# Kernel optimization log

Hardware: AMD Instinct MI355X
Metric: run time of the kernel (lower is better)

The kernel has to match this reference:

```python
import jax, jax.numpy as jnp
import numpy as np
from jax import lax

DECAY = 0.99
EPS = 1e-5


def setup_inputs() -> dict:
    key = jax.random.key(0)
    k1, k2, k3 = jax.random.split(key, 3)
    x = jax.random.normal(k1, (32, 64, 64, 64), dtype=jnp.float32)  # NCHW, C == embedding_dim
    embedding = jax.random.normal(k2, (512, 64), dtype=jnp.float32)  # [K, D] codebook
    cluster_size = jnp.ones((512,), dtype=jnp.float32)  # EMA buffer
    embedding_avg = jax.random.normal(k3, (512, 64), dtype=jnp.float32)  # EMA buffer
    return {"x": x, "embedding": embedding, "cluster_size": cluster_size, "embedding_avg": embedding_avg}


def reference(x, embedding, cluster_size, embedding_avg):
    n, c, h, w = x.shape
    K, D = embedding.shape
    # [N, D] flattened tokens (NHWC order, matching permute(0,2,3,1))
    flat_x = jnp.transpose(x, (0, 2, 3, 1)).reshape(-1, D)
    distances = (
        jnp.sum(flat_x ** 2, axis=1, keepdims=True)
        + jnp.sum(embedding ** 2, axis=1)
        - 2.0 * flat_x @ embedding.T
    )  # [N, K]
    idxs = jnp.argmin(distances, axis=1)  # [N]
    # one_hot @ embedding == gather (same math, no [N,K] one-hot GEMM)
    quantized = embedding[idxs].reshape(n, h, w, c)
    quantized = jnp.transpose(quantized, (0, 3, 1, 2))  # back to NCHW
    loss = jnp.mean((x - lax.stop_gradient(quantized)) ** 2)
    # EMA updates (training path). segment_sum == one_hot.sum(0) / flat_x.T @ one_hot
    ones = jnp.ones((flat_x.shape[0],), dtype=x.dtype)
    batch_cluster_size = jax.ops.segment_sum(ones, idxs, num_segments=K)  # [K]
    batch_embedding_avg = jax.ops.segment_sum(flat_x, idxs, num_segments=K)  # [K, D]
    new_cluster_size = cluster_size * DECAY + (1.0 - DECAY) * batch_cluster_size
    new_embedding_avg = embedding_avg * DECAY + (1.0 - DECAY) * batch_embedding_avg
    new_embedding = new_embedding_avg / (new_cluster_size + EPS)[:, None]
    # straight-through estimator
    quantized_st = x + lax.stop_gradient(quantized - x)
    return quantized_st, loss, new_embedding, new_cluster_size, new_embedding_avg
```

## Files before the change

kernel.cpp:

```cpp
#include <hip/hip_runtime.h>

#define HW 4096
#define KC 512

typedef __attribute__((ext_vector_type(8))) short s16x8;
typedef __attribute__((ext_vector_type(16))) float f32x16;

__device__ inline short f2bf(float f) {
    unsigned int u = __builtin_bit_cast(unsigned int, f);
    unsigned int lsb = (u >> 16) & 1u;
    u += 0x7fffu + lsb;
    return (short)(u >> 16);
}
__device__ inline float bf2f(short h) {
    unsigned int u = ((unsigned int)(unsigned short)h) << 16;
    return __builtin_bit_cast(float, u);
}

#define WS_EN    133136
#define WS_EHF   135184
#define WS_ELF   217104
#define WS_IDX   282640

__global__ void k_prep_en(const float* __restrict__ emb, float* __restrict__ en) {
    int m = blockIdx.x * 256 + threadIdx.x;
    if (m >= KC) return;
    const float* e = emb + m * 64;
    float d0 = 0.f, d1 = 0.f, d2 = 0.f, d3 = 0.f;
#pragma unroll
    for (int c = 0; c < 64; c += 4) {
        d0 = fmaf(e[c], e[c], d0);
        d1 = fmaf(e[c + 1], e[c + 1], d1);
        d2 = fmaf(e[c + 2], e[c + 2], d2);
        d3 = fmaf(e[c + 3], e[c + 3], d3);
    }
    en[m] = (d0 + d1) + (d2 + d3);
}

__global__ void k_prep_frag(const float* __restrict__ emb, const float* __restrict__ en,
                            short* __restrict__ ehf, short* __restrict__ elf) {
    int t = blockIdx.x * 256 + threadIdx.x;
    int m = t >> 3, ko = t & 7;
    int mt = m >> 5, ks = ko >> 1;
    int lane = (m & 31) + 32 * (ko & 1);
    s16x8 hv, lv;
#pragma unroll
    for (int j = 0; j < 8; ++j) {
        float v = emb[m * 64 + ko * 8 + j];
        short h = f2bf(v);
        hv[j] = h;
        lv[j] = f2bf(v - bf2f(h));
    }
    ((s16x8*)ehf)[(mt * 5 + ks) * 64 + lane] = hv;
    ((s16x8*)elf)[(mt * 4 + ks) * 64 + lane] = lv;

    int e2 = t * 2;
    int mt2 = e2 >> 9;
    int lane2 = (e2 >> 3) & 63;
    int j2 = e2 & 7;
    unsigned int val = 0;
    if (lane2 < 32 && j2 == 0) {
        float ev = en[mt2 * 32 + (lane2 & 31)];
        short eh_ = f2bf(ev);
        short el_ = f2bf(ev - bf2f(eh_));
        val = ((unsigned int)(unsigned short)eh_) | (((unsigned int)(unsigned short)el_) << 16);
    }
    *(unsigned int*)(ehf + ((size_t)(mt2 * 5 + 4) * 64 + lane2) * 8 + j2) = val;
}

__device__ inline void merge2(float& s1, int& i1, float& s2, int& i2,
                              float os1, int oi1, float os2, int oi2) {
    bool ob = (os1 < s1) || (os1 == s1 && oi1 < i1);
    float n1s = ob ? os1 : s1;  int n1i = ob ? oi1 : i1;
    float ls  = ob ? s1  : os1; int li  = ob ? i1  : oi1;
    float ws  = ob ? os2 : s2;  int wi  = ob ? oi2 : i2;
    bool b2 = (ls < ws) || (ls == ws && li < wi);
    s1 = n1s; i1 = n1i;
    s2 = b2 ? ls : ws; i2 = b2 ? li : wi;
}

__global__ __launch_bounds__(256) void k_main(const float* __restrict__ x,
                                              const short* __restrict__ ehf,
                                              const short* __restrict__ elf,
                                              const float* __restrict__ en,
                                              const float* __restrict__ emb,
                                              float* __restrict__ qout,
                                              unsigned short* __restrict__ idx_out,
                                              float* __restrict__ loss_acc) {
    int tid = threadIdx.x;
    int wv = tid >> 6, lane = tid & 63;
    int tb = blockIdx.x * 256;
    int n = tb >> 12, hwb = tb & 4095;
    const float* xp = x + (size_t)n * 64 * HW;
    int wbase = hwb + wv * 64;

    int l5 = lane & 31;
    int kh = (lane >> 5) * 8;

    s16x8 fah[5], fbh[5], fal[4], fbl[4];
    {
        const float* pa = xp + wbase + l5;
        const float* pb = pa + 32;
#pragma unroll
        for (int ks = 0; ks < 4; ++ks) {
            s16x8 ha, la, hb, lb;
#pragma unroll
            for (int j = 0; j < 8; ++j) {
                int c = ks * 16 + kh + j;
                float va = -2.0f * pa[(size_t)c * HW];
                float vb = -2.0f * pb[(size_t)c * HW];
                short h0 = f2bf(va); ha[j] = h0; la[j] = f2bf(va - bf2f(h0));
                short h1 = f2bf(vb); hb[j] = h1; lb[j] = f2bf(vb - bf2f(h1));
            }
            fah[ks] = ha; fal[ks] = la; fbh[ks] = hb; fbl[ks] = lb;
        }
        s16x8 v0;
#pragma unroll
        for (int j = 0; j < 8; ++j) v0[j] = 0;
        if (lane < 32) { v0[0] = (short)0x3F80; v0[1] = (short)0x3F80; }
        fah[4] = v0; fbh[4] = v0;
    }

    const s16x8* eh8 = (const s16x8*)ehf;
    const s16x8* el8 = (const s16x8*)elf;

    float s1a = 3.402823466e38f, s2a = 3.402823466e38f;
    float s1b = 3.402823466e38f, s2b = 3.402823466e38f;
    int i1a = 0, i2a = 0, i1b = 0, i2b = 0;
    int hv4 = (lane >> 5) * 4;

#pragma unroll 2
    for (int mt = 0; mt < 16; ++mt) {
        s16x8 ah[5], al[4];
#pragma unroll
        for (int ks = 0; ks < 5; ++ks) ah[ks] = eh8[(mt * 5 + ks) * 64 + lane];
#pragma unroll
        for (int ks = 0; ks < 4; ++ks) al[ks] = el8[(mt * 4 + ks) * 64 + lane];

        f32x16 acc0, acc1;
#pragma unroll
        for (int r = 0; r < 16; ++r) { acc0[r] = 0.0f; acc1[r] = 0.0f; }
#pragma unroll
        for (int ks = 0; ks < 5; ++ks) {
            acc0 = __builtin_amdgcn_mfma_f32_32x32x16_bf16(ah[ks], fah[ks], acc0, 0, 0, 0);
            acc1 = __builtin_amdgcn_mfma_f32_32x32x16_bf16(ah[ks], fbh[ks], acc1, 0, 0, 0);
        }
#pragma unroll
        for (int ks = 0; ks < 4; ++ks) {
            acc0 = __builtin_amdgcn_mfma_f32_32x32x16_bf16(al[ks], fah[ks], acc0, 0, 0, 0);
            acc1 = __builtin_amdgcn_mfma_f32_32x32x16_bf16(al[ks], fbh[ks], acc1, 0, 0, 0);
        }
#pragma unroll
        for (int ks = 0; ks < 4; ++ks) {
            acc0 = __builtin_amdgcn_mfma_f32_32x32x16_bf16(ah[ks], fal[ks], acc0, 0, 0, 0);
            acc1 = __builtin_amdgcn_mfma_f32_32x32x16_bf16(ah[ks], fbl[ks], acc1, 0, 0, 0);
        }

        int mb = mt * 32 + hv4;
#pragma unroll
        for (int r = 0; r < 16; ++r) {
            int mi = mb + (r & 3) + 8 * (r >> 2);
            {
                float s = acc0[r];
                bool c1 = s < s1a, c2 = s < s2a;
                s2a = c1 ? s1a : (c2 ? s : s2a); i2a = c1 ? i1a : (c2 ? mi : i2a);
                s1a = c1 ? s : s1a;              i1a = c1 ? mi : i1a;
            }
            {
                float s = acc1[r];
                bool c1 = s < s1b, c2 = s < s2b;
                s2b = c1 ? s1b : (c2 ? s : s2b); i2b = c1 ? i1b : (c2 ? mi : i2b);
                s1b = c1 ? s : s1b;              i1b = c1 ? mi : i1b;
            }
        }
    }

    merge2(s1a, i1a, s2a, i2a, __shfl_xor(s1a, 32), __shfl_xor(i1a, 32),
           __shfl_xor(s2a, 32), __shfl_xor(i2a, 32));
    merge2(s1b, i1b, s2b, i2b, __shfl_xor(s1b, 32), __shfl_xor(i1b, 32),
           __shfl_xor(s2b, 32), __shfl_xor(i2b, 32));

    bool hi = (lane & 32) != 0;
    int I1 = hi ? i1b : i1a;
    int I2 = hi ? i2b : i2a;

    int hw = wbase + lane;
    const float* xq = xp + hw;
    float xv[64];
#pragma unroll
    for (int c = 0; c < 64; ++c) xv[c] = xq[(size_t)c * HW];

    float sxx;
    {
        float d0 = 0.f, d1 = 0.f, d2 = 0.f, d3 = 0.f;
#pragma unroll
        for (int c = 0; c < 64; c += 4) {
            d0 = fmaf(xv[c], xv[c], d0);
            d1 = fmaf(xv[c + 1], xv[c + 1], d1);
            d2 = fmaf(xv[c + 2], xv[c + 2], d2);
            d3 = fmaf(xv[c + 3], xv[c + 3], d3);
        }
        sxx = (d0 + d1) + (d2 + d3);
    }

    int ia = (I1 < I2) ? I1 : I2;
    int ib = (I1 < I2) ? I2 : I1;
    float sa, sb;
    {
        const float4* er = (const float4*)(emb + (size_t)ia * 64);
        float d0 = 0.f, d1 = 0.f, d2 = 0.f, d3 = 0.f;
#pragma unroll
        for (int q = 0; q < 16; ++q) {
            float4 e4 = er[q];
            d0 = fmaf(xv[q * 4], e4.x, d0);
            d1 = fmaf(xv[q * 4 + 1], e4.y, d1);
            d2 = fmaf(xv[q * 4 + 2], e4.z, d2);
            d3 = fmaf(xv[q * 4 + 3], e4.w, d3);
        }
        sa = (sxx + en[ia]) - 2.0f * ((d0 + d1) + (d2 + d3));
    }
    {
        const float4* er = (const float4*)(emb + (size_t)ib * 64);
        float d0 = 0.f, d1 = 0.f, d2 = 0.f, d3 = 0.f;
#pragma unroll
        for (int q = 0; q < 16; ++q) {
            float4 e4 = er[q];
            d0 = fmaf(xv[q * 4], e4.x, d0);
            d1 = fmaf(xv[q * 4 + 1], e4.y, d1);
            d2 = fmaf(xv[q * 4 + 2], e4.z, d2);
            d3 = fmaf(xv[q * 4 + 3], e4.w, d3);
        }
        sb = (sxx + en[ib]) - 2.0f * ((d0 + d1) + (d2 + d3));
    }
    int win = (sb < sa) ? ib : ia;

    idx_out[tb + wv * 64 + lane] = (unsigned short)win;

    const float4* ew = (const float4*)(emb + (size_t)win * 64);
    float* qp = qout + (size_t)n * 64 * HW + hw;
    float l0 = 0.f, l1 = 0.f, l2 = 0.f, l3 = 0.f;
#pragma unroll
    for (int q = 0; q < 16; ++q) {
        float4 e4 = ew[q];
        qp[(size_t)(q * 4) * HW] = e4.x;
        qp[(size_t)(q * 4 + 1) * HW] = e4.y;
        qp[(size_t)(q * 4 + 2) * HW] = e4.z;
        qp[(size_t)(q * 4 + 3) * HW] = e4.w;
        float f0 = xv[q * 4] - e4.x, f1 = xv[q * 4 + 1] - e4.y;
        float f2 = xv[q * 4 + 2] - e4.z, f3 = xv[q * 4 + 3] - e4.w;
        l0 = fmaf(f0, f0, l0);
        l1 = fmaf(f1, f1, l1);
        l2 = fmaf(f2, f2, l2);
        l3 = fmaf(f3, f3, l3);
    }
    float lp = (l0 + l1) + (l2 + l3);
#pragma unroll
    for (int off = 32; off; off >>= 1) lp += __shfl_down(lp, off);
    if (lane == 0) atomicAdd(loss_acc, lp);
}

__global__ __launch_bounds__(1024) void k_seg(const float* __restrict__ x,
                                              const unsigned short* __restrict__ idx,
                                              float* __restrict__ cnt_g,
                                              float* __restrict__ avg_g) {
    __shared__ float acc[KC * 9];
    __shared__ float cnt[KC];
    int tid = threadIdx.x;
    int n = blockIdx.x >> 3;
    int cg = blockIdx.x & 7;

    for (int i = tid; i < KC * 9; i += 1024) acc[i] = 0.f;
    if (cg == 0 && tid < KC) cnt[tid] = 0.f;
    __syncthreads();

    const float* xp = x + (size_t)n * 64 * HW + (size_t)(cg * 8) * HW;
    const unsigned short* ip = idx + n * HW;

#pragma unroll
    for (int p = 0; p < 4; ++p) {
        int hw = p * 1024 + tid;
        int k = ip[hw];
        if (cg == 0) atomicAdd(&cnt[k], 1.0f);
        float* row = acc + k * 9;
#pragma unroll
        for (int j = 0; j < 8; ++j) {
            atomicAdd(&row[j], xp[(size_t)j * HW + hw]);
        }
    }
    __syncthreads();

    for (int i = tid; i < KC * 8; i += 1024) {
        int k = i >> 3, j = i & 7;
        atomicAdd(&avg_g[k * 64 + cg * 8 + j], acc[k * 9 + j]);
    }
    if (cg == 0 && tid < KC) atomicAdd(&cnt_g[tid], cnt[tid]);
}

__global__ void k_fin(const float* __restrict__ cs_in, const float* __restrict__ avg_in,
                      const float* __restrict__ cnt, const float* __restrict__ avgacc,
                      const float* __restrict__ loss_acc,
                      float* __restrict__ loss_out, float* __restrict__ emb_out,
                      float* __restrict__ cs_out, float* __restrict__ avg_out) {
    int i = blockIdx.x * 256 + threadIdx.x;
    if (i >= KC * 64) return;
    int k = i >> 6, c = i & 63;
    float ncs = cs_in[k] * 0.99f + 0.01f * cnt[k];
    float nav = avg_in[i] * 0.99f + 0.01f * avgacc[i];
    avg_out[i] = nav;
    emb_out[i] = nav / (ncs + 1e-5f);
    if (c == 0) cs_out[k] = ncs;
    if (i == 0) loss_out[0] = loss_acc[0] * (1.0f / 8388608.0f);
}

extern "C" void kernel_launch(void* const* d_in, const int* in_sizes, int n_in,
                              void* d_out, int out_size, void* d_ws, size_t ws_size,
                              hipStream_t stream) {
    (void)in_sizes; (void)n_in; (void)out_size; (void)ws_size;
    const float* x   = (const float*)d_in[0];
    const float* emb = (const float*)d_in[1];
    const float* cs  = (const float*)d_in[2];
    const float* avg = (const float*)d_in[3];

    float* out      = (float*)d_out;
    float* qout     = out;
    float* loss_out = out + 8388608;
    float* emb_out  = loss_out + 1;
    float* cs_out   = emb_out + 32768;
    float* avg_out  = cs_out + 512;

    char* wsb = (char*)d_ws;
    float* cnt_acc  = (float*)wsb;
    float* avg_acc  = (float*)(wsb + 2048);
    float* loss_acc = (float*)(wsb + 133120);
    float* en       = (float*)(wsb + WS_EN);
    short* ehf      = (short*)(wsb + WS_EHF);
    short* elf      = (short*)(wsb + WS_ELF);
    unsigned short* idx = (unsigned short*)(wsb + WS_IDX);

    hipMemsetAsync(d_ws, 0, 133124, stream);
    k_prep_en<<<2, 256, 0, stream>>>(emb, en);
    k_prep_frag<<<16, 256, 0, stream>>>(emb, en, ehf, elf);
    k_main<<<512, 256, 0, stream>>>(x, ehf, elf, en, emb, qout, idx, loss_acc);
    k_seg<<<256, 1024, 0, stream>>>(x, idx, cnt_acc, avg_acc);
    k_fin<<<128, 256, 0, stream>>>(cs, avg, cnt_acc, avg_acc, loss_acc,
                                   loss_out, emb_out, cs_out, avg_out);
}
```

Measured before the change: 158.0 us.

## Halve per-wave token tile in k_main and split refinement across half-waves

Each wave now handles 32 tokens instead of 64, using one MFMA accumulator instead of two, and the grid doubles to 1024 blocks with a launch bound of 4 blocks per CU. The rescoring and write-back phase splits the 64 channels between the two half-waves and combines partial dot products with a cross-lane shuffle, so each lane keeps 32 x values instead of 64. The aim is lower register pressure, higher occupancy and more blocks to hide memory latency. In exchange, every wave reloads the full codebook fragments for half as many tokens, doubling codebook fragment traffic per token, and the stores become 32-wide per channel row.

Result: slower. 229.7 us (+45.4%).

```diff
diff --git a/kernel.cpp b/kernel.cpp
--- a/kernel.cpp
+++ b/kernel.cpp
@@ -79,7 +79,7 @@
     s2 = b2 ? ls : ws; i2 = b2 ? li : wi;
 }
 
-__global__ __launch_bounds__(256) void k_main(const float* __restrict__ x,
+__global__ __launch_bounds__(256, 4) void k_main(const float* __restrict__ x,
                                               const short* __restrict__ ehf,
                                               const short* __restrict__ elf,
                                               const float* __restrict__ en,
@@ -89,44 +89,40 @@
                                               float* __restrict__ loss_acc) {
     int tid = threadIdx.x;
     int wv = tid >> 6, lane = tid & 63;
-    int tb = blockIdx.x * 256;
+    int tb = blockIdx.x * 128;
     int n = tb >> 12, hwb = tb & 4095;
     const float* xp = x + (size_t)n * 64 * HW;
-    int wbase = hwb + wv * 64;
+    int wbase = hwb + wv * 32;
 
     int l5 = lane & 31;
     int kh = (lane >> 5) * 8;
 
-    s16x8 fah[5], fbh[5], fal[4], fbl[4];
+    s16x8 fh[5], fl[4];
     {
         const float* pa = xp + wbase + l5;
-        const float* pb = pa + 32;
 #pragma unroll
         for (int ks = 0; ks < 4; ++ks) {
-            s16x8 ha, la, hb, lb;
+            s16x8 ha, la;
 #pragma unroll
             for (int j = 0; j < 8; ++j) {
                 int c = ks * 16 + kh + j;
                 float va = -2.0f * pa[(size_t)c * HW];
-                float vb = -2.0f * pb[(size_t)c * HW];
                 short h0 = f2bf(va); ha[j] = h0; la[j] = f2bf(va - bf2f(h0));
-                short h1 = f2bf(vb); hb[j] = h1; lb[j] = f2bf(vb - bf2f(h1));
             }
-            fah[ks] = ha; fal[ks] = la; fbh[ks] = hb; fbl[ks] = lb;
+            fh[ks] = ha; fl[ks] = la;
         }
         s16x8 v0;
 #pragma unroll
         for (int j = 0; j < 8; ++j) v0[j] = 0;
         if (lane < 32) { v0[0] = (short)0x3F80; v0[1] = (short)0x3F80; }
-        fah[4] = v0; fbh[4] = v0;
+        fh[4] = v0;
     }
 
     const s16x8* eh8 = (const s16x8*)ehf;
     const s16x8* el8 = (const s16x8*)elf;
 
-    float s1a = 3.402823466e38f, s2a = 3.402823466e38f;
-    float s1b = 3.402823466e38f, s2b = 3.402823466e38f;
-    int i1a = 0, i2a = 0, i1b = 0, i2b = 0;
+    float s1 = 3.402823466e38f, s2 = 3.402823466e38f;
+    int i1 = 0, i2 = 0;
     int hv4 = (lane >> 5) * 4;
 
 #pragma unroll 2
@@ -137,117 +133,107 @@
 #pragma unroll
         for (int ks = 0; ks < 4; ++ks) al[ks] = el8[(mt * 4 + ks) * 64 + lane];
 
-        f32x16 acc0, acc1;
-#pragma unroll
-        for (int r = 0; r < 16; ++r) { acc0[r] = 0.0f; acc1[r] = 0.0f; }
-#pragma unroll
-        for (int ks = 0; ks < 5; ++ks) {
-            acc0 = __builtin_amdgcn_mfma_f32_32x32x16_bf16(ah[ks], fah[ks], acc0, 0, 0, 0);
-            acc1 = __builtin_amdgcn_mfma_f32_32x32x16_bf16(ah[ks], fbh[ks], acc1, 0, 0, 0);
-        }
-#pragma unroll
-        for (int ks = 0; ks < 4; ++ks) {
-            acc0 = __builtin_amdgcn_mfma_f32_32x32x16_bf16(al[ks], fah[ks], acc0, 0, 0, 0);
-            acc1 = __builtin_amdgcn_mfma_f32_32x32x16_bf16(al[ks], fbh[ks], acc1, 0, 0, 0);
-        }
-#pragma unroll
-        for (int ks = 0; ks < 4; ++ks) {
-            acc0 = __builtin_amdgcn_mfma_f32_32x32x16_bf16(ah[ks], fal[ks], acc0, 0, 0, 0);
-            acc1 = __builtin_amdgcn_mfma_f32_32x32x16_bf16(ah[ks], fbl[ks], acc1, 0, 0, 0);
-        }
+        f32x16 acc;
+#pragma unroll
+        for (int r = 0; r < 16; ++r) acc[r] = 0.0f;
+#pragma unroll
+        for (int ks = 0; ks < 5; ++ks)
+            acc = __builtin_amdgcn_mfma_f32_32x32x16_bf16(ah[ks], fh[ks], acc, 0, 0, 0);
+#pragma unroll
+        for (int ks = 0; ks < 4; ++ks)
+            acc = __builtin_amdgcn_mfma_f32_32x32x16_bf16(al[ks], fh[ks], acc, 0, 0, 0);
+#pragma unroll
+        for (int ks = 0; ks < 4; ++ks)
+            acc = __builtin_amdgcn_mfma_f32_32x32x16_bf16(ah[ks], fl[ks], acc, 0, 0, 0);
 
         int mb = mt * 32 + hv4;
 #pragma unroll
         for (int r = 0; r < 16; ++r) {
             int mi = mb + (r & 3) + 8 * (r >> 2);
-            {
-                float s = acc0[r];
-                bool c1 = s < s1a, c2 = s < s2a;
-                s2a = c1 ? s1a : (c2 ? s : s2a); i2a = c1 ? i1a : (c2 ? mi : i2a);
-                s1a = c1 ? s : s1a;              i1a = c1 ? mi : i1a;
-            }
-            {
-                float s = acc1[r];
-                bool c1 = s < s1b, c2 = s < s2b;
-                s2b = c1 ? s1b : (c2 ? s : s2b); i2b = c1 ? i1b : (c2 ? mi : i2b);
-                s1b = c1 ? s : s1b;              i1b = c1 ? mi : i1b;
-            }
-        }
-    }
-
-    merge2(s1a, i1a, s2a, i2a, __shfl_xor(s1a, 32), __shfl_xor(i1a, 32),
-           __shfl_xor(s2a, 32), __shfl_xor(i2a, 32));
-    merge2(s1b, i1b, s2b, i2b, __shfl_xor(s1b, 32), __shfl_xor(i1b, 32),
-           __shfl_xor(s2b, 32), __shfl_xor(i2b, 32));
-
-    bool hi = (lane & 32) != 0;
-    int I1 = hi ? i1b : i1a;
-    int I2 = hi ? i2b : i2a;
-
-    int hw = wbase + lane;
-    const float* xq = xp + hw;
-    float xv[64];
-#pragma unroll
-    for (int c = 0; c < 64; ++c) xv[c] = xq[(size_t)c * HW];
+            float s = acc[r];
+            bool c1 = s < s1, c2 = s < s2;
+            s2 = c1 ? s1 : (c2 ? s : s2); i2 = c1 ? i1 : (c2 ? mi : i2);
+            s1 = c1 ? s : s1;             i1 = c1 ? mi : i1;
+        }
+    }
+
+    merge2(s1, i1, s2, i2, __shfl_xor(s1, 32), __shfl_xor(i1, 32),
+           __shfl_xor(s2, 32), __shfl_xor(i2, 32));
+
+    int ia = (i1 < i2) ? i1 : i2;
+    int ib = (i1 < i2) ? i2 : i1;
+
+    int coff = (lane >> 5) * 32;
+    const float* xq = xp + wbase + l5;
+    float xh[32];
+#pragma unroll
+    for (int j = 0; j < 32; ++j) xh[j] = xq[(size_t)(coff + j) * HW];
 
     float sxx;
     {
         float d0 = 0.f, d1 = 0.f, d2 = 0.f, d3 = 0.f;
 #pragma unroll
-        for (int c = 0; c < 64; c += 4) {
-            d0 = fmaf(xv[c], xv[c], d0);
-            d1 = fmaf(xv[c + 1], xv[c + 1], d1);
-            d2 = fmaf(xv[c + 2], xv[c + 2], d2);
-            d3 = fmaf(xv[c + 3], xv[c + 3], d3);
-        }
-        sxx = (d0 + d1) + (d2 + d3);
-    }
-
-    int ia = (I1 < I2) ? I1 : I2;
-    int ib = (I1 < I2) ? I2 : I1;
-    float sa, sb;
+        for (int j = 0; j < 32; j += 4) {
+            d0 = fmaf(xh[j], xh[j], d0);
+            d1 = fmaf(xh[j + 1], xh[j + 1], d1);
+            d2 = fmaf(xh[j + 2], xh[j + 2], d2);
+            d3 = fmaf(xh[j + 3], xh[j + 3], d3);
+        }
+        float part = (d0 + d1) + (d2 + d3);
+        float oth = __shfl_xor(part, 32);
+        sxx = (lane < 32) ? (part + oth) : (oth + part);
+    }
+
+    float da, db;
     {
-        const float4* er = (const float4*)(emb + (size_t)ia * 64);
+        const float4* er = (const float4*)(emb + (size_t)ia * 64) + (coff >> 2);
         float d0 = 0.f, d1 = 0.f, d2 = 0.f, d3 = 0.f;
 #pragma unroll
-        for (int q = 0; q < 16; ++q) {
+        for (int q = 0; q < 8; ++q) {
             float4 e4 = er[q];
-            d0 = fmaf(xv[q * 4], e4.x, d0);
-            d1 = fmaf(xv[q * 4 + 1], e4.y, d1);
-            d2 = fmaf(xv[q * 4 + 2], e4.z, d2);
-            d3 = fmaf(xv[q * 4 + 3], e4.w, d3);
-        }
-        sa = (sxx + en[ia]) - 2.0f * ((d0 + d1) + (d2 + d3));
+            d0 = fmaf(xh[q * 4], e4.x, d0);
+            d1 = fmaf(xh[q * 4 + 1], e4.y, d1);
+            d2 = fmaf(xh[q * 4 + 2], e4.z, d2);
+            d3 = fmaf(xh[q * 4 + 3], e4.w, d3);
+        }
+        float part = (d0 + d1) + (d2 + d3);
+        float oth = __shfl_xor(part, 32);
+        da = (lane < 32) ? (part + oth) : (oth + part);
     }
     {
-        const float4* er = (const float4*)(emb + (size_t)ib * 64);
+        const float4* er = (const float4*)(emb + (size_t)ib * 64) + (coff >> 2);
         float d0 = 0.f, d1 = 0.f, d2 = 0.f, d3 = 0.f;
 #pragma unroll
-        for (int q = 0; q < 16; ++q) {
+        for (int q = 0; q < 8; ++q) {
             float4 e4 = er[q];
-            d0 = fmaf(xv[q * 4], e4.x, d0);
-            d1 = fmaf(xv[q * 4 + 1], e4.y, d1);
-            d2 = fmaf(xv[q * 4 + 2], e4.z, d2);
-            d3 = fmaf(xv[q * 4 + 3], e4.w, d3);
-        }
-        sb = (sxx + en[ib]) - 2.0f * ((d0 + d1) + (d2 + d3));
-    }
+            d0 = fmaf(xh[q * 4], e4.x, d0);
+            d1 = fmaf(xh[q * 4 + 1], e4.y, d1);
+            d2 = fmaf(xh[q * 4 + 2], e4.z, d2);
+            d3 = fmaf(xh[q * 4 + 3], e4.w, d3);
+        }
+        float part = (d0 + d1) + (d2 + d3);
+        float oth = __shfl_xor(part, 32);
+        db = (lane < 32) ? (part + oth) : (oth + part);
+    }
+    float sa = (sxx + en[ia]) - 2.0f * da;
+    float sb = (sxx + en[ib]) - 2.0f * db;
     int win = (sb < sa) ? ib : ia;
 
-    idx_out[tb + wv * 64 + lane] = (unsigned short)win;
-
-    const float4* ew = (const float4*)(emb + (size_t)win * 64);
-    float* qp = qout + (size_t)n * 64 * HW + hw;
+    if (lane < 32) idx_out[tb + wv * 32 + l5] = (unsigned short)win;
+
+    const float4* ew = (const float4*)(emb + (size_t)win * 64) + (coff >> 2);
+    float* qp = qout + (size_t)n * 64 * HW + wbase + l5;
     float l0 = 0.f, l1 = 0.f, l2 = 0.f, l3 = 0.f;
 #pragma unroll
-    for (int q = 0; q < 16; ++q) {
+    for (int q = 0; q < 8; ++q) {
         float4 e4 = ew[q];
-        qp[(size_t)(q * 4) * HW] = e4.x;
-        qp[(size_t)(q * 4 + 1) * HW] = e4.y;
-        qp[(size_t)(q * 4 + 2) * HW] = e4.z;
-        qp[(size_t)(q * 4 + 3) * HW] = e4.w;
-        float f0 = xv[q * 4] - e4.x, f1 = xv[q * 4 + 1] - e4.y;
-        float f2 = xv[q * 4 + 2] - e4.z, f3 = xv[q * 4 + 3] - e4.w;
+        int c = coff + q * 4;
+        qp[(size_t)c * HW] = e4.x;
+        qp[(size_t)(c + 1) * HW] = e4.y;
+        qp[(size_t)(c + 2) * HW] = e4.z;
+        qp[(size_t)(c + 3) * HW] = e4.w;
+        float f0 = xh[q * 4] - e4.x, f1 = xh[q * 4 + 1] - e4.y;
+        float f2 = xh[q * 4 + 2] - e4.z, f3 = xh[q * 4 + 3] - e4.w;
         l0 = fmaf(f0, f0, l0);
         l1 = fmaf(f1, f1, l1);
         l2 = fmaf(f2, f2, l2);
@@ -340,7 +326,7 @@
     hipMemsetAsync(d_ws, 0, 133124, stream);
     k_prep_en<<<2, 256, 0, stream>>>(emb, en);
     k_prep_frag<<<16, 256, 0, stream>>>(emb, en, ehf, elf);
-    k_main<<<512, 256, 0, stream>>>(x, ehf, elf, en, emb, qout, idx, loss_acc);
+    k_main<<<1024, 256, 0, stream>>>(x, ehf, elf, en, emb, qout, idx, loss_acc);
     k_seg<<<256, 1024, 0, stream>>>(x, idx, cnt_acc, avg_acc);
     k_fin<<<128, 256, 0, stream>>>(cs, avg, cnt_acc, avg_acc, loss_acc,
                                    loss_out, emb_out, cs_out, avg_out);
```

## Stage codebook fragments in LDS and split segment-sum blocks over halves

Applied to the files above, without the earlier changes.

k_main now runs 512-thread blocks that first copy the whole bf16 hi/lo codebook fragment tables (about 147KB) into shared memory, then read MFMA A-operands from LDS instead of global/L2. k_seg's grid is doubled, with each block handling half of the spatial positions, to raise parallelism. The LDS staging adds a per-block copy and a barrier. At roughly 147KB per block it may limit occupancy to one block per CU, which conflicts with the launch_bounds(512,2) hint. Running k_main on 256 blocks also reduces the block count relative to the CUs.

Result: faster. 139.5 us (-11.7%).

```diff
diff --git a/kernel.cpp b/kernel.cpp
--- a/kernel.cpp
+++ b/kernel.cpp
@@ -79,7 +79,7 @@
     s2 = b2 ? ls : ws; i2 = b2 ? li : wi;
 }
 
-__global__ __launch_bounds__(256) void k_main(const float* __restrict__ x,
+__global__ __launch_bounds__(512, 2) void k_main(const float* __restrict__ x,
                                               const short* __restrict__ ehf,
                                               const short* __restrict__ elf,
                                               const float* __restrict__ en,
@@ -87,12 +87,26 @@
                                               float* __restrict__ qout,
                                               unsigned short* __restrict__ idx_out,
                                               float* __restrict__ loss_acc) {
+    __shared__ short shH[16 * 5 * 64 * 8];
+    __shared__ short shL[16 * 4 * 64 * 8];
+
     int tid = threadIdx.x;
     int wv = tid >> 6, lane = tid & 63;
-    int tb = blockIdx.x * 256;
+    int tb = blockIdx.x * 512;
     int n = tb >> 12, hwb = tb & 4095;
     const float* xp = x + (size_t)n * 64 * HW;
     int wbase = hwb + wv * 64;
+
+    {
+        const s16x8* ehg = (const s16x8*)ehf;
+        const s16x8* elg = (const s16x8*)elf;
+        s16x8* sH = (s16x8*)shH;
+        s16x8* sL = (s16x8*)shL;
+#pragma unroll
+        for (int i = 0; i < 10; ++i) sH[i * 512 + tid] = ehg[i * 512 + tid];
+#pragma unroll
+        for (int i = 0; i < 8; ++i) sL[i * 512 + tid] = elg[i * 512 + tid];
+    }
 
     int l5 = lane & 31;
     int kh = (lane >> 5) * 8;
@@ -121,8 +135,10 @@
         fah[4] = v0; fbh[4] = v0;
     }
 
-    const s16x8* eh8 = (const s16x8*)ehf;
-    const s16x8* el8 = (const s16x8*)elf;
+    __syncthreads();
+
+    const s16x8* sH8 = (const s16x8*)shH;
+    const s16x8* sL8 = (const s16x8*)shL;
 
     float s1a = 3.402823466e38f, s2a = 3.402823466e38f;
     float s1b = 3.402823466e38f, s2b = 3.402823466e38f;
@@ -133,9 +149,9 @@
     for (int mt = 0; mt < 16; ++mt) {
         s16x8 ah[5], al[4];
 #pragma unroll
-        for (int ks = 0; ks < 5; ++ks) ah[ks] = eh8[(mt * 5 + ks) * 64 + lane];
-#pragma unroll
-        for (int ks = 0; ks < 4; ++ks) al[ks] = el8[(mt * 4 + ks) * 64 + lane];
+        for (int ks = 0; ks < 5; ++ks) ah[ks] = sH8[(mt * 5 + ks) * 64 + lane];
+#pragma unroll
+        for (int ks = 0; ks < 4; ++ks) al[ks] = sL8[(mt * 4 + ks) * 64 + lane];
 
         f32x16 acc0, acc1;
 #pragma unroll
@@ -266,18 +282,20 @@
     __shared__ float acc[KC * 9];
     __shared__ float cnt[KC];
     int tid = threadIdx.x;
-    int n = blockIdx.x >> 3;
-    int cg = blockIdx.x & 7;
+    int b = blockIdx.x;
+    int n = b >> 4;
+    int cg = (b >> 1) & 7;
+    int h = b & 1;
 
     for (int i = tid; i < KC * 9; i += 1024) acc[i] = 0.f;
     if (cg == 0 && tid < KC) cnt[tid] = 0.f;
     __syncthreads();
 
-    const float* xp = x + (size_t)n * 64 * HW + (size_t)(cg * 8) * HW;
-    const unsigned short* ip = idx + n * HW;
-
-#pragma unroll
-    for (int p = 0; p < 4; ++p) {
+    const float* xp = x + (size_t)n * 64 * HW + (size_t)(cg * 8) * HW + h * 2048;
+    const unsigned short* ip = idx + n * HW + h * 2048;
+
+#pragma unroll
+    for (int p = 0; p < 2; ++p) {
         int hw = p * 1024 + tid;
         int k = ip[hw];
         if (cg == 0) atomicAdd(&cnt[k], 1.0f);
@@ -340,8 +358,8 @@
     hipMemsetAsync(d_ws, 0, 133124, stream);
     k_prep_en<<<2, 256, 0, stream>>>(emb, en);
     k_prep_frag<<<16, 256, 0, stream>>>(emb, en, ehf, elf);
-    k_main<<<512, 256, 0, stream>>>(x, ehf, elf, en, emb, qout, idx, loss_acc);
-    k_seg<<<256, 1024, 0, stream>>>(x, idx, cnt_acc, avg_acc);
+    k_main<<<256, 512, 0, stream>>>(x, ehf, elf, en, emb, qout, idx, loss_acc);
+    k_seg<<<512, 1024, 0, stream>>>(x, idx, cnt_acc, avg_acc);
     k_fin<<<128, 256, 0, stream>>>(cs, avg, cnt_acc, avg_acc, loss_acc,
                                    loss_out, emb_out, cs_out, avg_out);
 }
```

## Split fused argmin/quantize kernel into separate argmin and quantize kernels

Applied to the files above, without the earlier changes.

The fused main kernel becomes two kernels. The argmin kernel has each wave handle 32 tokens with a single MFMA accumulator and launches twice as many blocks, writing the top-2 candidate codes per token to workspace. A separate quantize kernel then rescores the two candidates in fp32, writes the output and loss, and stores the winning index. The segment-sum kernel is split across twice as many blocks, each covering half the spatial positions, to raise parallelism. The price is an extra launch and x being read one more time, in exchange for more waves and less register pressure in the MFMA phase.

New measurement: 168.8 us. 1.07x slower.

```diff
diff --git a/kernel.cpp b/kernel.cpp
--- a/kernel.cpp
+++ b/kernel.cpp
@@ -20,7 +20,7 @@
 #define WS_EN    133136
 #define WS_EHF   135184
 #define WS_ELF   217104
-#define WS_IDX   282640
+#define WS_CAND  282640
 
 __global__ void k_prep_en(const float* __restrict__ emb, float* __restrict__ en) {
     int m = blockIdx.x * 256 + threadIdx.x;
@@ -79,54 +79,46 @@
     s2 = b2 ? ls : ws; i2 = b2 ? li : wi;
 }
 
-__global__ __launch_bounds__(256) void k_main(const float* __restrict__ x,
-                                              const short* __restrict__ ehf,
-                                              const short* __restrict__ elf,
-                                              const float* __restrict__ en,
-                                              const float* __restrict__ emb,
-                                              float* __restrict__ qout,
-                                              unsigned short* __restrict__ idx_out,
-                                              float* __restrict__ loss_acc) {
+__global__ __launch_bounds__(256) void k_argmin(const float* __restrict__ x,
+                                                const short* __restrict__ ehf,
+                                                const short* __restrict__ elf,
+                                                unsigned int* __restrict__ cand) {
     int tid = threadIdx.x;
     int wv = tid >> 6, lane = tid & 63;
-    int tb = blockIdx.x * 256;
+    int tb = blockIdx.x * 128;
     int n = tb >> 12, hwb = tb & 4095;
     const float* xp = x + (size_t)n * 64 * HW;
-    int wbase = hwb + wv * 64;
+    int wbase = hwb + wv * 32;
 
     int l5 = lane & 31;
     int kh = (lane >> 5) * 8;
 
-    s16x8 fah[5], fbh[5], fal[4], fbl[4];
+    s16x8 fh[5], fl[4];
     {
         const float* pa = xp + wbase + l5;
-        const float* pb = pa + 32;
 #pragma unroll
         for (int ks = 0; ks < 4; ++ks) {
-            s16x8 ha, la, hb, lb;
+            s16x8 ha, la;
 #pragma unroll
             for (int j = 0; j < 8; ++j) {
                 int c = ks * 16 + kh + j;
                 float va = -2.0f * pa[(size_t)c * HW];
-                float vb = -2.0f * pb[(size_t)c * HW];
                 short h0 = f2bf(va); ha[j] = h0; la[j] = f2bf(va - bf2f(h0));
-                short h1 = f2bf(vb); hb[j] = h1; lb[j] = f2bf(vb - bf2f(h1));
             }
-            fah[ks] = ha; fal[ks] = la; fbh[ks] = hb; fbl[ks] = lb;
+            fh[ks] = ha; fl[ks] = la;
         }
         s16x8 v0;
 #pragma unroll
         for (int j = 0; j < 8; ++j) v0[j] = 0;
         if (lane < 32) { v0[0] = (short)0x3F80; v0[1] = (short)0x3F80; }
-        fah[4] = v0; fbh[4] = v0;
+        fh[4] = v0;
     }
 
     const s16x8* eh8 = (const s16x8*)ehf;
     const s16x8* el8 = (const s16x8*)elf;
 
-    float s1a = 3.402823466e38f, s2a = 3.402823466e38f;
-    float s1b = 3.402823466e38f, s2b = 3.402823466e38f;
-    int i1a = 0, i2a = 0, i1b = 0, i2b = 0;
+    float s1 = 3.402823466e38f, s2 = 3.402823466e38f;
+    int i1 = 0, i2 = 0;
     int hv4 = (lane >> 5) * 4;
 
 #pragma unroll 2
@@ -137,58 +129,55 @@
 #pragma unroll
         for (int ks = 0; ks < 4; ++ks) al[ks] = el8[(mt * 4 + ks) * 64 + lane];
 
-        f32x16 acc0, acc1;
-#pragma unroll
-        for (int r = 0; r < 16; ++r) { acc0[r] = 0.0f; acc1[r] = 0.0f; }
-#pragma unroll
-        for (int ks = 0; ks < 5; ++ks) {
-            acc0 = __builtin_amdgcn_mfma_f32_32x32x16_bf16(ah[ks], fah[ks], acc0, 0, 0, 0);
-            acc1 = __builtin_amdgcn_mfma_f32_32x32x16_bf16(ah[ks], fbh[ks], acc1, 0, 0, 0);
-        }
-#pragma unroll
-        for (int ks = 0; ks < 4; ++ks) {
-            acc0 = __builtin_amdgcn_mfma_f32_32x32x16_bf16(al[ks], fah[ks], acc0, 0, 0, 0);
-            acc1 = __builtin_amdgcn_mfma_f32_32x32x16_bf16(al[ks], fbh[ks], acc1, 0, 0, 0);
-        }
-#pragma unroll
-        for (int ks = 0; ks < 4; ++ks) {
-            acc0 = __builtin_amdgcn_mfma_f32_32x32x16_bf16(ah[ks], fal[ks], acc0, 0, 0, 0);
-            acc1 = __builtin_amdgcn_mfma_f32_32x32x16_bf16(ah[ks], fbl[ks], acc1, 0, 0, 0);
-        }
+        f32x16 acc;
+#pragma unroll
+        for (int r = 0; r < 16; ++r) acc[r] = 0.0f;
+#pragma unroll
+        for (int ks = 0; ks < 5; ++ks)
+            acc = __builtin_amdgcn_mfma_f32_32x32x16_bf16(ah[ks], fh[ks], acc, 0, 0, 0);
+#pragma unroll
+        for (int ks = 0; ks < 4; ++ks)
+            acc = __builtin_amdgcn_mfma_f32_32x32x16_bf16(al[ks], fh[ks], acc, 0, 0, 0);
+#pragma unroll
+        for (int ks = 0; ks < 4; ++ks)
+            acc = __builtin_amdgcn_mfma_f32_32x32x16_bf16(ah[ks], fl[ks], acc, 0, 0, 0);
 
         int mb = mt * 32 + hv4;
 #pragma unroll
         for (int r = 0; r < 16; ++r) {
             int mi = mb + (r & 3) + 8 * (r >> 2);
-            {
-                float s = acc0[r];
-                bool c1 = s < s1a, c2 = s < s2a;
-                s2a = c1 ? s1a : (c2 ? s : s2a); i2a = c1 ? i1a : (c2 ? mi : i2a);
-                s1a = c1 ? s : s1a;              i1a = c1 ? mi : i1a;
-            }
-            {
-                float s = acc1[r];
-                bool c1 = s < s1b, c2 = s < s2b;
-                s2b = c1 ? s1b : (c2 ? s : s2b); i2b = c1 ? i1b : (c2 ? mi : i2b);
-                s1b = c1 ? s : s1b;              i1b = c1 ? mi : i1b;
-            }
-        }
-    }
-
-    merge2(s1a, i1a, s2a, i2a, __shfl_xor(s1a, 32), __shfl_xor(i1a, 32),
-           __shfl_xor(s2a, 32), __shfl_xor(i2a, 32));
-    merge2(s1b, i1b, s2b, i2b, __shfl_xor(s1b, 32), __shfl_xor(i1b, 32),
-           __shfl_xor(s2b, 32), __shfl_xor(i2b, 32));
-
-    bool hi = (lane & 32) != 0;
-    int I1 = hi ? i1b : i1a;
-    int I2 = hi ? i2b : i2a;
-
-    int hw = wbase + lane;
-    const float* xq = xp + hw;
+            float s = acc[r];
+            bool c1 = s < s1, c2 = s < s2;
+            s2 = c1 ? s1 : (c2 ? s : s2); i2 = c1 ? i1 : (c2 ? mi : i2);
+            s1 = c1 ? s : s1;             i1 = c1 ? mi : i1;
+        }
+    }
+
+    merge2(s1, i1, s2, i2, __shfl_xor(s1, 32), __shfl_xor(i1, 32),
+           __shfl_xor(s2, 32), __shfl_xor(i2, 32));
+
+    if (lane < 32)
+        cand[tb + wv * 32 + l5] = (unsigned int)i1 | ((unsigned int)i2 << 16);
+}
+
+__global__ __launch_bounds__(256) void k_quant(const float* __restrict__ x,
+                                               const float* __restrict__ emb,
+                                               const float* __restrict__ en,
+                                               unsigned int* __restrict__ cand,
+                                               float* __restrict__ qout,
+                                               float* __restrict__ loss_acc) {
+    int t = blockIdx.x * 256 + threadIdx.x;
+    int n = t >> 12, hw = t & 4095;
+    const float* xq = x + (size_t)n * 64 * HW + hw;
+
     float xv[64];
 #pragma unroll
     for (int c = 0; c < 64; ++c) xv[c] = xq[(size_t)c * HW];
+
+    unsigned int cd = cand[t];
+    int c1 = (int)(cd & 0xffffu), c2 = (int)(cd >> 16);
+    int ia = (c1 < c2) ? c1 : c2;
+    int ib = (c1 < c2) ? c2 : c1;
 
     float sxx;
     {
@@ -203,8 +192,6 @@
         sxx = (d0 + d1) + (d2 + d3);
     }
 
-    int ia = (I1 < I2) ? I1 : I2;
-    int ib = (I1 < I2) ? I2 : I1;
     float sa, sb;
     {
         const float4* er = (const float4*)(emb + (size_t)ia * 64);
@@ -233,8 +220,7 @@
         sb = (sxx + en[ib]) - 2.0f * ((d0 + d1) + (d2 + d3));
     }
     int win = (sb < sa) ? ib : ia;
-
-    idx_out[tb + wv * 64 + lane] = (unsigned short)win;
+    cand[t] = (unsigned int)win;
 
     const float4* ew = (const float4*)(emb + (size_t)win * 64);
     float* qp = qout + (size_t)n * 64 * HW + hw;
@@ -256,30 +242,32 @@
     float lp = (l0 + l1) + (l2 + l3);
 #pragma unroll
     for (int off = 32; off; off >>= 1) lp += __shfl_down(lp, off);
-    if (lane == 0) atomicAdd(loss_acc, lp);
+    if ((threadIdx.x & 63) == 0) atomicAdd(loss_acc, lp);
 }
 
 __global__ __launch_bounds__(1024) void k_seg(const float* __restrict__ x,
-                                              const unsigned short* __restrict__ idx,
+                                              const unsigned int* __restrict__ idx,
                                               float* __restrict__ cnt_g,
                                               float* __restrict__ avg_g) {
     __shared__ float acc[KC * 9];
     __shared__ float cnt[KC];
     int tid = threadIdx.x;
-    int n = blockIdx.x >> 3;
-    int cg = blockIdx.x & 7;
+    int b = blockIdx.x;
+    int n = b >> 4;
+    int cg = (b >> 1) & 7;
+    int h = b & 1;
 
     for (int i = tid; i < KC * 9; i += 1024) acc[i] = 0.f;
     if (cg == 0 && tid < KC) cnt[tid] = 0.f;
     __syncthreads();
 
-    const float* xp = x + (size_t)n * 64 * HW + (size_t)(cg * 8) * HW;
-    const unsigned short* ip = idx + n * HW;
-
-#pragma unroll
-    for (int p = 0; p < 4; ++p) {
+    const float* xp = x + (size_t)n * 64 * HW + (size_t)(cg * 8) * HW + h * 2048;
+    const unsigned int* ip = idx + n * HW + h * 2048;
+
+#pragma unroll
+    for (int p = 0; p < 2; ++p) {
         int hw = p * 1024 + tid;
-        int k = ip[hw];
+        int k = (int)ip[hw];
         if (cg == 0) atomicAdd(&cnt[k], 1.0f);
         float* row = acc + k * 9;
 #pragma unroll
@@ -335,13 +323,14 @@
     float* en       = (float*)(wsb + WS_EN);
     short* ehf      = (short*)(wsb + WS_EHF);
     short* elf      = (short*)(wsb + WS_ELF);
-    unsigned short* idx = (unsigned short*)(wsb + WS_IDX);
+    unsigned int* cand = (unsigned int*)(wsb + WS_CAND);
 
     hipMemsetAsync(d_ws, 0, 133124, stream);
     k_prep_en<<<2, 256, 0, stream>>>(emb, en);
     k_prep_frag<<<16, 256, 0, stream>>>(emb, en, ehf, elf);
-    k_main<<<512, 256, 0, stream>>>(x, ehf, elf, en, emb, qout, idx, loss_acc);
-    k_seg<<<256, 1024, 0, stream>>>(x, idx, cnt_acc, avg_acc);
+    k_argmin<<<1024, 256, 0, stream>>>(x, ehf, elf, cand);
+    k_quant<<<512, 256, 0, stream>>>(x, emb, en, cand, qout, loss_acc);
+    k_seg<<<512, 1024, 0, stream>>>(x, cand, cnt_acc, avg_acc);
     k_fin<<<128, 256, 0, stream>>>(cs, avg, cnt_acc, avg_acc, loss_acc,
                                    loss_out, emb_out, cs_out, avg_out);
 }
```
